# Kernel optimization log

Measured on AMD Instinct MI355X. Metric: run time of the kernel, lower is better.

The kernel has to match this reference:

```python
import jax, jax.numpy as jnp
import numpy as np


def _rms(x, w=None, eps=1e-6):
    # RMSNorm in fp32 like the torch module, optional elementwise affine.
    x32 = x.astype(jnp.float32)
    r = jax.lax.rsqrt(jnp.mean(x32 * x32, axis=-1, keepdims=True) + eps)
    y = (x32 * r).astype(x.dtype)
    return y * w if w is not None else y


def _rotate_half(x):
    x1, x2 = jnp.split(x, 2, axis=-1)
    return jnp.concatenate([-x2, x1], axis=-1)


def setup_inputs() -> dict:
    key = jax.random.key(0)
    ks = jax.random.split(key, 10)
    B, N, C, H = 16, 1024, 1152, 16
    hd = C // H          # 72
    hid = 3072           # _swiglu_hidden(1152, 4.0)
    grid = 32            # grid**2 == N
    quarter = hd // 4    # 18
    # exact axial RoPE cache (build_axial_rope_cache)
    inv_freq = 1.0 / (10000.0 ** (np.arange(quarter, dtype=np.float32) / quarter))
    pos = np.arange(grid, dtype=np.float32)
    f1 = pos[:, None] * inv_freq[None, :]                               # (grid, quarter)
    fy = np.broadcast_to(f1[:, None, :], (grid, grid, quarter)).reshape(-1, quarter)
    fx = np.broadcast_to(f1[None, :, :], (grid, grid, quarter)).reshape(-1, quarter)

    def cs(f):
        e = np.concatenate([f, f], axis=-1)                             # (N, hd//2)
        return jnp.asarray(np.cos(e))[None, None], jnp.asarray(np.sin(e))[None, None]

    cos_y, sin_y = cs(fy)
    cos_x, sin_x = cs(fx)

    def w(k, shp, scale=0.02):
        return jax.random.normal(k, shp, jnp.float32) * scale

    return {
        "x": jax.random.normal(ks[0], (B, N, C), jnp.float32),
        "temb": jax.random.normal(ks[1], (B, C), jnp.float32),
        "cos_y": cos_y, "sin_y": sin_y, "cos_x": cos_x, "sin_x": sin_x,
        "Wqkv": w(ks[2], (3 * C, C)), "bqkv": jnp.zeros((3 * C,), jnp.float32),
        "Wt": w(ks[3], (3 * C, C)), "bt": jnp.zeros((3 * C,), jnp.float32),
        "Wp": w(ks[4], (C, C)), "bp": jnp.zeros((C,), jnp.float32),
        "qn_w": jnp.ones((hd,), jnp.float32), "kn_w": jnp.ones((hd,), jnp.float32),
        "Wg": w(ks[5], (hid, C)), "bg": jnp.zeros((hid,), jnp.float32),
        "Wu": w(ks[6], (hid, C)), "bu": jnp.zeros((hid,), jnp.float32),
        "Wd": w(ks[7], (C, hid)), "bd": jnp.zeros((C,), jnp.float32),
    }


def reference(x, temb, cos_y, sin_y, cos_x, sin_x, Wqkv, bqkv, Wt, bt, Wp, bp,
              qn_w, kn_w, Wg, bg, Wu, bu, Wd, bd):
    B, N, C = x.shape
    H = 16
    hd = C // H

    # --- TMSA attention branch ---
    xn = _rms(x)                                            # norm1 (no affine)
    qkv = xn @ Wqkv.T + bqkv + (temb @ Wt.T + bt)[:, None, :]
    qkv = qkv.reshape(B, N, 3, H, hd).transpose(2, 0, 3, 1, 4)  # (3,B,H,N,hd)
    q, k, v = qkv[0], qkv[1], qkv[2]
    q = _rms(q, qn_w)
    k = _rms(k, kn_w)

    def rope(t):
        ty, tx = jnp.split(t, 2, axis=-1)
        ty = ty * cos_y + _rotate_half(ty) * sin_y
        tx = tx * cos_x + _rotate_half(tx) * sin_x
        return jnp.concatenate([ty, tx], axis=-1)

    q, k = rope(q), rope(k)

    scores = jnp.einsum('bhnd,bhmd->bhnm', q, k) / jnp.sqrt(jnp.float32(hd))
    attn = jax.nn.softmax(scores, axis=-1)
    o = jnp.einsum('bhnm,bhmd->bhnd', attn, v)
    o = o.transpose(0, 2, 1, 3).reshape(B, N, C)
    x = x + (o @ Wp.T + bp)

    # --- SwiGLU MLP branch ---
    xn2 = _rms(x)                                           # norm2 (no affine)
    h = jax.nn.silu(xn2 @ Wg.T + bg) * (xn2 @ Wu.T + bu)
    x = x + (h @ Wd.T + bd)
    return x
```

## Files before the change

kernel.cpp:

```cpp
#include <hip/hip_runtime.h>
#include <cstdint>
#include <cstddef>

typedef unsigned short u16;
typedef unsigned int u32;
typedef __attribute__((ext_vector_type(8))) short bf16x8s;
typedef __attribute__((ext_vector_type(4))) float f32x4;

#define ASG __attribute__((address_space(1)))
#define ASL __attribute__((address_space(3)))

__device__ __forceinline__ u16 f2bf(float f){
  union { float f; unsigned u; } v; v.f = f;
  unsigned r = v.u + 0x7FFFu + ((v.u >> 16) & 1u);
  return (u16)(r >> 16);
}
__device__ __forceinline__ float bf2f(u16 h){
  union { unsigned u; float f; } v; v.u = ((unsigned)h) << 16;
  return v.f;
}

__global__ __launch_bounds__(256) void cvt_kernel(const float* __restrict__ in,
                                                  u16* __restrict__ out, int n){
  int i = blockIdx.x*256 + threadIdx.x;
  if (i < n) out[i] = f2bf(in[i]);
}

__global__ __launch_bounds__(256) void cvt_gu_kernel(const float* __restrict__ Wg,
                                                     const float* __restrict__ Wu,
                                                     u16* __restrict__ out){
  size_t i = (size_t)blockIdx.x*256 + threadIdx.x;
  if (i >= (size_t)6144*1152) return;
  int j = (int)(i / 1152), k = (int)(i % 1152);
  int b16 = j >> 4, w = j & 15;
  int src = (b16 >> 1)*16 + w;
  const float* W = (b16 & 1) ? Wu : Wg;
  out[i] = f2bf(W[(size_t)src*1152 + k]);
}

__global__ __launch_bounds__(256) void temb_kernel(const float* __restrict__ temb,
                                                   const float* __restrict__ Wt,
                                                   const float* __restrict__ bt,
                                                   const float* __restrict__ bqkv,
                                                   float* __restrict__ tvec){
  const int col  = blockIdx.x*4 + (threadIdx.x>>6);
  const int lane = threadIdx.x & 63;
  const float* wp = Wt + (size_t)col*1152;
  float w[18];
  #pragma unroll
  for (int j=0;j<18;j++) w[j] = wp[lane + j*64];
  float acc[16];
  #pragma unroll
  for (int b=0;b<16;b++) acc[b] = 0.f;
  #pragma unroll
  for (int j=0;j<18;j++){
    const int k = lane + j*64;
    #pragma unroll
    for (int b=0;b<16;b++) acc[b] += w[j]*temb[b*1152 + k];
  }
  #pragma unroll
  for (int b=0;b<16;b++){
    #pragma unroll
    for (int d=1; d<64; d<<=1) acc[b] += __shfl_xor(acc[b], d);
  }
  if (lane == 0){
    float add = bt[col] + bqkv[col];
    #pragma unroll
    for (int b=0;b<16;b++) tvec[(size_t)b*3456 + col] = acc[b] + add;
  }
}

__global__ __launch_bounds__(256) void rms_kernel(const float* __restrict__ in,
                                                  u16* __restrict__ out, int C){
  int row = blockIdx.x;
  const float* p = in + (size_t)row*C;
  float ss = 0.f;
  for (int c = threadIdx.x; c < C; c += 256){ float v = p[c]; ss += v*v; }
  #pragma unroll
  for (int d=1; d<64; d<<=1) ss += __shfl_xor(ss, d);
  __shared__ float wsum[4];
  if ((threadIdx.x & 63) == 0) wsum[threadIdx.x>>6] = ss;
  __syncthreads();
  float tot = wsum[0]+wsum[1]+wsum[2]+wsum[3];
  float r = rsqrtf(tot/(float)C + 1e-6f);
  u16* o = out + (size_t)row*C;
  for (int c = threadIdx.x; c < C; c += 256) o[c] = f2bf(p[c]*r);
}

template<int MODE>
__global__ __launch_bounds__(512, 4) void gemm_kernel(
    const u16* __restrict__ A, const u16* __restrict__ B,
    int M, int N, int K, int nbx, int segw,
    const float* __restrict__ bias, const float* __restrict__ fextra,
    void* __restrict__ outv, u16* __restrict__ out2, u16* __restrict__ out3)
{
  __shared__ __align__(16) u16 As0[256*32];
  __shared__ __align__(16) u16 As1[256*32];
  __shared__ __align__(16) u16 As2[256*32];
  __shared__ __align__(16) u16 Bs0[128*32];
  __shared__ __align__(16) u16 Bs1[128*32];
  __shared__ __align__(16) u16 Bs2[128*32];
  const int tid  = threadIdx.x;
  const int lane = tid & 63;
  const int wv   = tid >> 6;
  const int wr   = wv >> 1, wc = wv & 1;

  const int nwg  = (int)gridDim.x;
  const int bid  = (int)blockIdx.x;
  const int xcd  = bid & 7;
  const int slot = bid >> 3;
  const int mdep = (nwg >> 3) / nbx;
  const int segsz = mdep * segw;
  const int seg  = slot / segsz;
  const int rem  = slot - seg*segsz;
  const int mi   = rem / segw;
  const int ni   = seg*segw + (rem - mi*segw);
  const long m0 = (long)(xcd*mdep + mi) * 256;
  const long n0 = (long)ni * 128;

  const u16* Ab = A + (size_t)m0*K;
  const u16* Bb = B + (size_t)n0*K;

  const int gsw  = ((lane&3) ^ ((lane>>3)&3)) * 8;
  const int srow = lane >> 2;

  f32x4 acc[4][4];
  #pragma unroll
  for (int i=0;i<4;i++)
    #pragma unroll
    for (int j=0;j<4;j++) acc[i][j] = (f32x4){0.f,0.f,0.f,0.f};

  auto stage = [&](u16* as, u16* bs, int kt){
    __builtin_amdgcn_global_load_lds(
      (const ASG void*)(Ab + (size_t)(wv*16 + srow)*K + kt + gsw),
      (ASL void*)(as + wv*512), 16, 0, 0);
    __builtin_amdgcn_global_load_lds(
      (const ASG void*)(Ab + (size_t)(128 + wv*16 + srow)*K + kt + gsw),
      (ASL void*)(as + 4096 + wv*512), 16, 0, 0);
    __builtin_amdgcn_global_load_lds(
      (const ASG void*)(Bb + (size_t)(wv*16 + srow)*K + kt + gsw),
      (ASL void*)(bs + wv*512), 16, 0, 0);
  };
  auto compute = [&](const u16* as, const u16* bs){
    const int swc = (((lane>>4) ^ ((lane>>1)&3))) * 8;
    const int lc16 = lane & 15;
    bf16x8s af[4], bfr[4];
    #pragma unroll
    for (int i=0;i<4;i++)
      af[i] = *(const bf16x8s*)(as + (wr*64 + i*16 + lc16)*32 + swc);
    #pragma unroll
    for (int j=0;j<4;j++)
      bfr[j] = *(const bf16x8s*)(bs + (wc*64 + j*16 + lc16)*32 + swc);
    #pragma unroll
    for (int i=0;i<4;i++)
      #pragma unroll
      for (int j=0;j<4;j++)
        acc[i][j] = __builtin_amdgcn_mfma_f32_16x16x32_bf16(af[i], bfr[j], acc[i][j], 0,0,0);
  };

  const int NT = K >> 5;
  stage(As0, Bs0, 0);
  stage(As1, Bs1, 32);
  asm volatile("s_waitcnt vmcnt(3)" ::: "memory");
  __builtin_amdgcn_s_barrier();
  __builtin_amdgcn_sched_barrier(0);

  for (int t = 0; t < NT; t += 3){
    if (t+2 < NT) stage(As2, Bs2, (t+2)*32);
    compute(As0, Bs0);
    if (t+2 < NT) asm volatile("s_waitcnt vmcnt(3)" ::: "memory");
    else          asm volatile("s_waitcnt vmcnt(0)" ::: "memory");
    __builtin_amdgcn_s_barrier();
    __builtin_amdgcn_sched_barrier(0);
    if (t+3 < NT) stage(As0, Bs0, (t+3)*32);
    compute(As1, Bs1);
    if (t+3 < NT) asm volatile("s_waitcnt vmcnt(3)" ::: "memory");
    else          asm volatile("s_waitcnt vmcnt(0)" ::: "memory");
    __builtin_amdgcn_s_barrier();
    __builtin_amdgcn_sched_barrier(0);
    if (t+4 < NT) stage(As1, Bs1, (t+4)*32);
    compute(As2, Bs2);
    if (t+4 < NT) asm volatile("s_waitcnt vmcnt(3)" ::: "memory");
    else          asm volatile("s_waitcnt vmcnt(0)" ::: "memory");
    __builtin_amdgcn_s_barrier();
    __builtin_amdgcn_sched_barrier(0);
  }

  const int lr = (lane>>4)*4, lc = lane&15;
  #pragma unroll
  for (int i=0;i<4;i++){
    #pragma unroll
    for (int j=0;j<4;j++){
      long colg = n0 + wc*64 + j*16 + lc;
      long rowg0 = m0 + wr*64 + i*16 + lr;
      if (MODE==0){
        int cg = (int)colg;
        int which = cg / 1152;
        int rem2 = cg - which*1152;
        int hh = rem2 / 72, dd = rem2 - hh*72;
        int b = (int)(rowg0 >> 10), n = (int)(rowg0 & 1023);
        size_t bh = (size_t)(b*16 + hh);
        float tadd = fextra[(size_t)b*3456 + colg];
        if (which == 2){
          ushort4 vv;
          vv.x = f2bf(acc[i][j][0] + tadd);
          vv.y = f2bf(acc[i][j][1] + tadd);
          vv.z = f2bf(acc[i][j][2] + tadd);
          vv.w = f2bf(acc[i][j][3] + tadd);
          *(ushort4*)(out3 + (bh*72 + dd)*1024 + n) = vv;
        } else {
          u16* dst = (which==0) ? (u16*)outv : out2;
          #pragma unroll
          for (int r=0;r<4;r++)
            dst[(bh*1024 + (size_t)(n + r))*72 + dd] = f2bf(acc[i][j][r] + tadd);
        }
      } else {
        #pragma unroll
        for (int r=0;r<4;r++){
          long rowg = rowg0 + r;
          float v = acc[i][j][r];
          size_t oi = (size_t)rowg*N + colg;
          v += bias[colg] + fextra[oi];
          ((float*)outv)[oi] = v;
        }
      }
    }
  }
}

template<int MODE>
__global__ __launch_bounds__(256, 3) void gemm_half(
    const u16* __restrict__ A, const u16* __restrict__ B,
    int M, int N, int K, int nbx, int segw,
    const float* __restrict__ bias, const float* __restrict__ fextra,
    float* __restrict__ outv)
{
  __shared__ __align__(16) u16 As0[128*32];
  __shared__ __align__(16) u16 As1[128*32];
  __shared__ __align__(16) u16 As2[128*32];
  __shared__ __align__(16) u16 Bs0[128*32];
  __shared__ __align__(16) u16 Bs1[128*32];
  __shared__ __align__(16) u16 Bs2[128*32];
  const int tid  = threadIdx.x;
  const int lane = tid & 63;
  const int wv   = tid >> 6;
  const int wr   = wv >> 1, wc = wv & 1;

  const int nwg  = (int)gridDim.x;
  const int bid  = (int)blockIdx.x;
  const int xcd  = bid & 7;
  const int slot = bid >> 3;
  const int mdep = (nwg >> 3) / nbx;
  const int segsz = mdep * segw;
  const int seg  = slot / segsz;
  const int rem  = slot - seg*segsz;
  const int mi   = rem / segw;
  const int ni   = seg*segw + (rem - mi*segw);
  const long m0 = (long)(xcd*mdep + mi) * 128;
  const long n0 = (long)ni * 128;

  const u16* Ab = A + (size_t)m0*K;
  const u16* Bb = B + (size_t)n0*K;

  const int gsw  = ((lane&3) ^ ((lane>>3)&3)) * 8;
  const int srow = lane >> 2;

  f32x4 acc[4][4];
  #pragma unroll
  for (int i=0;i<4;i++)
    #pragma unroll
    for (int j=0;j<4;j++) acc[i][j] = (f32x4){0.f,0.f,0.f,0.f};

  auto stage = [&](u16* as, u16* bs, int kt){
    __builtin_amdgcn_global_load_lds(
      (const ASG void*)(Ab + (size_t)(wv*16 + srow)*K + kt + gsw),
      (ASL void*)(as + wv*512), 16, 0, 0);
    __builtin_amdgcn_global_load_lds(
      (const ASG void*)(Ab + (size_t)(64 + wv*16 + srow)*K + kt + gsw),
      (ASL void*)(as + 2048 + wv*512), 16, 0, 0);
    __builtin_amdgcn_global_load_lds(
      (const ASG void*)(Bb + (size_t)(wv*16 + srow)*K + kt + gsw),
      (ASL void*)(bs + wv*512), 16, 0, 0);
    __builtin_amdgcn_global_load_lds(
      (const ASG void*)(Bb + (size_t)(64 + wv*16 + srow)*K + kt + gsw),
      (ASL void*)(bs + 2048 + wv*512), 16, 0, 0);
  };
  auto compute = [&](const u16* as, const u16* bs){
    const int swc = (((lane>>4) ^ ((lane>>1)&3))) * 8;
    const int lc16 = lane & 15;
    bf16x8s af[4], bfr[4];
    #pragma unroll
    for (int i=0;i<4;i++)
      af[i] = *(const bf16x8s*)(as + (wr*64 + i*16 + lc16)*32 + swc);
    #pragma unroll
    for (int j=0;j<4;j++)
      bfr[j] = *(const bf16x8s*)(bs + (wc*64 + j*16 + lc16)*32 + swc);
    #pragma unroll
    for (int i=0;i<4;i++)
      #pragma unroll
      for (int j=0;j<4;j++)
        acc[i][j] = __builtin_amdgcn_mfma_f32_16x16x32_bf16(af[i], bfr[j], acc[i][j], 0,0,0);
  };

  const int NT = K >> 5;
  stage(As0, Bs0, 0);
  stage(As1, Bs1, 32);
  asm volatile("s_waitcnt vmcnt(4)" ::: "memory");
  __builtin_amdgcn_s_barrier();
  __builtin_amdgcn_sched_barrier(0);

  for (int t = 0; t < NT; t += 3){
    if (t+2 < NT) stage(As2, Bs2, (t+2)*32);
    compute(As0, Bs0);
    if (t+2 < NT) asm volatile("s_waitcnt vmcnt(4)" ::: "memory");
    else          asm volatile("s_waitcnt vmcnt(0)" ::: "memory");
    __builtin_amdgcn_s_barrier();
    __builtin_amdgcn_sched_barrier(0);
    if (t+3 < NT) stage(As0, Bs0, (t+3)*32);
    compute(As1, Bs1);
    if (t+3 < NT) asm volatile("s_waitcnt vmcnt(4)" ::: "memory");
    else          asm volatile("s_waitcnt vmcnt(0)" ::: "memory");
    __builtin_amdgcn_s_barrier();
    __builtin_amdgcn_sched_barrier(0);
    if (t+4 < NT) stage(As1, Bs1, (t+4)*32);
    compute(As2, Bs2);
    if (t+4 < NT) asm volatile("s_waitcnt vmcnt(4)" ::: "memory");
    else          asm volatile("s_waitcnt vmcnt(0)" ::: "memory");
    __builtin_amdgcn_s_barrier();
    __builtin_amdgcn_sched_barrier(0);
  }

  const int lr = (lane>>4)*4, lc = lane&15;
  #pragma unroll
  for (int i=0;i<4;i++){
    #pragma unroll
    for (int j=0;j<4;j++){
      long colg = n0 + wc*64 + j*16 + lc;
      long rowg0 = m0 + wr*64 + i*16 + lr;
      #pragma unroll
      for (int r=0;r<4;r++){
        long rowg = rowg0 + r;
        size_t oi = (size_t)rowg*N + colg;
        outv[oi] = acc[i][j][r] + bias[colg] + fextra[oi];
      }
    }
  }
}

__global__ __launch_bounds__(512, 2) void gemm_gu8(
    const u16* __restrict__ A, const u16* __restrict__ B,
    int K, int nbx, int segw,
    const float* __restrict__ bg, const float* __restrict__ bu,
    u16* __restrict__ out)
{
  __shared__ __align__(16) u16 As0[256*64];
  __shared__ __align__(16) u16 Bs0[256*64];
  __shared__ __align__(16) u16 As1[256*64];
  __shared__ __align__(16) u16 Bs1[256*64];
  const int tid  = threadIdx.x;
  const int lane = tid & 63;
  const int wv   = tid >> 6;
  const int wr   = wv >> 2;
  const int wc   = wv & 3;
  const int g = lane >> 4, c = lane & 15;

  const int nwg  = (int)gridDim.x;
  const int bid  = (int)blockIdx.x;
  const int xcd  = bid & 7;
  const int slot = bid >> 3;
  const int mdep = (nwg >> 3) / nbx;
  const int segsz = mdep * segw;
  const int seg  = slot / segsz;
  const int rem  = slot - seg*segsz;
  const int mi   = rem / segw;
  const int ni   = seg*segw + (rem - mi*segw);
  const long m0 = (long)(xcd*mdep + mi) * 256;
  const long n0 = (long)ni * 256;

  const u16* Ab = A + (size_t)m0*K;
  const u16* Bb = B + (size_t)n0*K;

  const int srow = tid >> 3;
  const int q8   = ((tid & 7) ^ (srow & 7)) * 8;

  auto stageTo = [&](u16* dst, const u16* src, int h, int kt){
    __builtin_amdgcn_global_load_lds(
      (const ASG void*)(src + (size_t)(h*128 + srow)*K + kt + q8),
      (ASL void*)(dst + h*8192 + wv*512), 16, 0, 0);
    __builtin_amdgcn_global_load_lds(
      (const ASG void*)(src + (size_t)(h*128 + 64 + srow)*K + kt + q8),
      (ASL void*)(dst + h*8192 + 4096 + wv*512), 16, 0, 0);
  };

  f32x4 acc[8][4];
  #pragma unroll
  for (int i=0;i<8;i++)
    #pragma unroll
    for (int j=0;j<4;j++) acc[i][j] = (f32x4){0.f,0.f,0.f,0.f};

  const int sw0 = ((g     ) ^ (c & 7)) * 16;
  const int sw1 = ((4 + g ) ^ (c & 7)) * 16;

  const int NT = K >> 6;

  stageTo(As0, Ab, 0, 0);  stageTo(As0, Ab, 1, 0);
  stageTo(Bs0, Bb, 0, 0);  stageTo(Bs0, Bb, 1, 0);
  stageTo(Bs1, Bb, 0, 64); stageTo(Bs1, Bb, 1, 64);
  asm volatile("s_waitcnt vmcnt(4)" ::: "memory");
  __builtin_amdgcn_s_barrier();
  __builtin_amdgcn_sched_barrier(0);

  auto ktile = [&](const u16* CA, u16* CB, u16* NA, int t){
    const char* aB = (const char*)CA + wr*16384;
    const char* bB = (const char*)CB + (wc>>1)*16384;
    bf16x8s bfr[4][2];
    #pragma unroll
    for (int p=0;p<4;p++){
      const int r0 = (2*p)*16 + c;
      const int r1 = r0 + 16;
      bf16x8s a00 = *(const bf16x8s*)(aB + r0*128 + sw0);
      bf16x8s a01 = *(const bf16x8s*)(aB + r0*128 + sw1);
      bf16x8s a10 = *(const bf16x8s*)(aB + r1*128 + sw0);
      bf16x8s a11 = *(const bf16x8s*)(aB + r1*128 + sw1);
      if (p==0){
        #pragma unroll
        for (int j=0;j<4;j++){
          const int br = (wc&1)*64 + j*16 + c;
          bfr[j][0] = *(const bf16x8s*)(bB + br*128 + sw0);
          bfr[j][1] = *(const bf16x8s*)(bB + br*128 + sw1);
        }
        if (t+1 < NT) stageTo(NA, Ab, 0, (t+1)*64);
      } else if (p==1){
        if (t+1 < NT) stageTo(NA, Ab, 1, (t+1)*64);
      } else if (p==2){
        if (t+2 < NT) stageTo(CB, Bb, 0, (t+2)*64);
      } else {
        if (t+2 < NT) stageTo(CB, Bb, 1, (t+2)*64);
      }
      __builtin_amdgcn_s_barrier();
      asm volatile("s_waitcnt lgkmcnt(0)" ::: "memory");
      __builtin_amdgcn_sched_barrier(0);
      __builtin_amdgcn_s_setprio(1);
      #pragma unroll
      for (int j=0;j<4;j++){
        acc[2*p  ][j] = __builtin_amdgcn_mfma_f32_16x16x32_bf16(a00, bfr[j][0], acc[2*p  ][j],0,0,0);
        acc[2*p  ][j] = __builtin_amdgcn_mfma_f32_16x16x32_bf16(a01, bfr[j][1], acc[2*p  ][j],0,0,0);
        acc[2*p+1][j] = __builtin_amdgcn_mfma_f32_16x16x32_bf16(a10, bfr[j][0], acc[2*p+1][j],0,0,0);
        acc[2*p+1][j] = __builtin_amdgcn_mfma_f32_16x16x32_bf16(a11, bfr[j][1], acc[2*p+1][j],0,0,0);
      }
      __builtin_amdgcn_s_setprio(0);
      if (p==3){
        if (t+2 < NT) asm volatile("s_waitcnt vmcnt(4)" ::: "memory");
        else          asm volatile("s_waitcnt vmcnt(0)" ::: "memory");
      }
      __builtin_amdgcn_s_barrier();
      __builtin_amdgcn_sched_barrier(0);
    }
  };

  for (int tp = 0; tp < NT; tp += 2){
    ktile(As0, Bs0, As1, tp);
    ktile(As1, Bs1, As0, tp+1);
  }

  #pragma unroll
  for (int i=0;i<8;i++){
    #pragma unroll
    for (int jp=0;jp<2;jp++){
      long hcol = (n0>>1) + wc*32 + jp*16 + c;
      float bgv = bg[hcol], buv = bu[hcol];
      #pragma unroll
      for (int r=0;r<4;r++){
        long rowg = m0 + wr*128 + i*16 + g*4 + r;
        float gv = acc[i][2*jp  ][r] + bgv;
        float uv = acc[i][2*jp+1][r] + buv;
        float hv = (gv/(1.f + __expf(-gv))) * uv;
        out[(size_t)rowg*3072 + hcol] = f2bf(hv);
      }
    }
  }
}

__global__ __launch_bounds__(256) void qkrope_kernel(
    u16* __restrict__ Q, u16* __restrict__ K,
    const float* __restrict__ qn_w, const float* __restrict__ kn_w,
    const float* __restrict__ cos_y, const float* __restrict__ sin_y,
    const float* __restrict__ cos_x, const float* __restrict__ sin_x)
{
  const int gw   = blockIdx.x*4 + (threadIdx.x>>6);
  const int lane = threadIdx.x & 63;
  const int n = gw & 1023;
  const int d0 = lane*2;
  const bool act = d0 < 72;
  const float scale = 0.11785113019775793f;

  u16* qp = Q + (size_t)gw*72;
  u16* kp = K + (size_t)gw*72;
  float q0=0,q1=0,k0=0,k1=0,wq0=0,wq1=0,wk0=0,wk1=0;
  if (act){
    q0 = bf2f(qp[d0]); q1 = bf2f(qp[d0+1]);
    k0 = bf2f(kp[d0]); k1 = bf2f(kp[d0+1]);
    wq0 = qn_w[d0]; wq1 = qn_w[d0+1];
    wk0 = kn_w[d0]; wk1 = kn_w[d0+1];
  }
  float ssq = q0*q0 + q1*q1;
  float ssk = k0*k0 + k1*k1;
  #pragma unroll
  for (int d=1; d<64; d<<=1){ ssq += __shfl_xor(ssq,d); ssk += __shfl_xor(ssk,d); }
  const float rq = rsqrtf(ssq*(1.f/72.f) + 1e-6f);
  const float rk = rsqrtf(ssk*(1.f/72.f) + 1e-6f);
  float qn0 = q0*rq*wq0, qn1 = q1*rq*wq1;
  float kn0 = k0*rk*wk0, kn1 = k1*rk*wk1;

  int dh = d0 % 36;
  const bool first = (dh < 18);
  int partner = first ? lane+9 : lane-9;
  if (!act) partner = lane;
  float pq0 = __shfl(qn0, partner), pq1 = __shfl(qn1, partner);
  float pk0 = __shfl(kn0, partner), pk1 = __shfl(kn1, partner);
  if (act){
    const float* cp = (d0 < 36) ? cos_y : cos_x;
    const float* sp = (d0 < 36) ? sin_y : sin_x;
    float c0 = cp[n*36+dh], c1 = cp[n*36+dh+1];
    float s0 = sp[n*36+dh], s1 = sp[n*36+dh+1];
    float sgn = first ? -1.f : 1.f;
    float qo0 = (qn0*c0 + sgn*pq0*s0)*scale, qo1 = (qn1*c1 + sgn*pq1*s1)*scale;
    float ko0 = kn0*c0 + sgn*pk0*s0,         ko1 = kn1*c1 + sgn*pk1*s1;
    *(unsigned*)(qp + d0) = (unsigned)f2bf(qo0) | ((unsigned)f2bf(qo1)<<16);
    *(unsigned*)(kp + d0) = (unsigned)f2bf(ko0) | ((unsigned)f2bf(ko1)<<16);
  }
}

__global__ __launch_bounds__(256, 3) void attn_kernel(
    const u16* __restrict__ Q, const u16* __restrict__ K,
    const u16* __restrict__ Vt, u16* __restrict__ O)
{
  const int tid  = threadIdx.x;
  const int lane = tid & 63;
  const int wv   = tid >> 6;
  const int g = lane >> 4, c = lane & 15;
  const int bid  = blockIdx.x;
  const int head = (bid >> 6) * 8 + (bid & 7);
  const int q0   = ((bid >> 3) & 7) * 128;
  const int b = head >> 4, h = head & 15;

  __shared__ __align__(16) u16 Vlds[80][72];
  __shared__ __align__(16) u16 Plds[8][16][64];

  const bf16x8s zf = {0,0,0,0,0,0,0,0};
  const u16* Kp = K + (size_t)head*1024*72;
  const u16* Qb = Q + ((size_t)head*1024 + q0 + wv*32)*72;
  const char* Vg = (const char*)(Vt + (size_t)head*72*1024);

  bf16x8s qf[2][3];
  #pragma unroll
  for (int s=0;s<2;s++){
    const u16* qrow = Qb + (size_t)(s*16 + c)*72;
    qf[s][0] = *(const bf16x8s*)(qrow + g*8);
    qf[s][1] = *(const bf16x8s*)(qrow + 32 + g*8);
    qf[s][2] = (g==0) ? *(const bf16x8s*)(qrow + 64) : zf;
  }

  f32x4 oacc[2][5];
  float lsum[2] = {0.f, 0.f};
  #pragma unroll
  for (int s=0;s<2;s++)
    #pragma unroll
    for (int c5=0;c5<5;c5++) oacc[s][c5] = (f32x4){0.f,0.f,0.f,0.f};

  char* pb0 = (char*)Plds + (wv*2+0)*2048 + c*128;
  char* pb1 = pb0 + 2048;
  const int swz = (c & 7) << 4;

  int4 vr0, vr1, vr2;
  {
    vr0 = *(const int4*)(Vg + ((tid    )>>3)*2048 + ((tid    )&7)*16);
    vr1 = *(const int4*)(Vg + ((256+tid)>>3)*2048 + ((256+tid)&7)*16);
    if (tid < 64) vr2 = *(const int4*)(Vg + ((512+tid)>>3)*2048 + ((512+tid)&7)*16);
  }
  if (tid < 288) ((u32*)&Vlds[72][0])[tid] = 0u;
  {
    *(int4*)((char*)Vlds + ((tid    )>>3)*144 + ((tid    )&7)*16) = vr0;
    *(int4*)((char*)Vlds + ((256+tid)>>3)*144 + ((256+tid)&7)*16) = vr1;
    if (tid < 64) *(int4*)((char*)Vlds + ((512+tid)>>3)*144 + ((512+tid)&7)*16) = vr2;
  }

  for (int t = 0; t < 16; ++t){
    const int kv0 = t*64;
    __syncthreads();
    if (t < 15){
      const char* vs = Vg + (kv0+64)*2;
      vr0 = *(const int4*)(vs + ((tid    )>>3)*2048 + ((tid    )&7)*16);
      vr1 = *(const int4*)(vs + ((256+tid)>>3)*2048 + ((256+tid)&7)*16);
      if (tid < 64) vr2 = *(const int4*)(vs + ((512+tid)>>3)*2048 + ((512+tid)&7)*16);
    }

    #pragma unroll
    for (int nf=0; nf<4; nf++){
      const u16* krow = Kp + (size_t)(kv0 + nf*16 + c)*72;
      bf16x8s kf0 = *(const bf16x8s*)(krow + g*8);
      bf16x8s kf1 = *(const bf16x8s*)(krow + 32 + g*8);
      bf16x8s kf2 = (g==0) ? *(const bf16x8s*)(krow + 64) : zf;
      #pragma unroll
      for (int s=0;s<2;s++){
        f32x4 sc = (f32x4){0.f,0.f,0.f,0.f};
        sc = __builtin_amdgcn_mfma_f32_16x16x32_bf16(kf0, qf[s][0], sc,0,0,0);
        sc = __builtin_amdgcn_mfma_f32_16x16x32_bf16(kf1, qf[s][1], sc,0,0,0);
        sc = __builtin_amdgcn_mfma_f32_16x16x32_bf16(kf2, qf[s][2], sc,0,0,0);
        float p0 = __expf(sc[0]), p1 = __expf(sc[1]);
        float p2 = __expf(sc[2]), p3 = __expf(sc[3]);
        lsum[s] += (p0+p1) + (p2+p3);
        u32 w0 = (u32)f2bf(p0) | ((u32)f2bf(p1) << 16);
        u32 w1 = (u32)f2bf(p2) | ((u32)f2bf(p3) << 16);
        char* pb = s ? pb1 : pb0;
        int kb = nf*32 + g*8;
        *(u32*)(pb + ( kb      ^ swz)) = w0;
        *(u32*)(pb + ((kb + 4) ^ swz)) = w1;
      }
    }
    asm volatile("" ::: "memory");
    bf16x8s pa[2][2];
    #pragma unroll
    for (int s=0;s<2;s++)
      #pragma unroll
      for (int w2=0;w2<2;w2++)
        pa[s][w2] = *(const bf16x8s*)((s?pb1:pb0) + ((w2*64 + g*16) ^ swz));

    #pragma unroll
    for (int c5=0;c5<5;c5++){
      #pragma unroll
      for (int w2=0;w2<2;w2++){
        bf16x8s vf = *(const bf16x8s*)((const char*)Vlds + (size_t)(c5*16+c)*144 + w2*64 + g*16);
        oacc[0][c5] = __builtin_amdgcn_mfma_f32_16x16x32_bf16(pa[0][w2], vf, oacc[0][c5],0,0,0);
        oacc[1][c5] = __builtin_amdgcn_mfma_f32_16x16x32_bf16(pa[1][w2], vf, oacc[1][c5],0,0,0);
      }
    }

    if (t < 15){
      __syncthreads();
      *(int4*)((char*)Vlds + ((tid    )>>3)*144 + ((tid    )&7)*16) = vr0;
      *(int4*)((char*)Vlds + ((256+tid)>>3)*144 + ((256+tid)&7)*16) = vr1;
      if (tid < 64) *(int4*)((char*)Vlds + ((512+tid)>>3)*144 + ((512+tid)&7)*16) = vr2;
    }
  }

  size_t obase = (size_t)b*1024*1152 + (size_t)h*72;
  #pragma unroll
  for (int s=0;s<2;s++){
    float ls = lsum[s];
    ls += __shfl_xor(ls, 16);
    ls += __shfl_xor(ls, 32);
    float linv[4];
    #pragma unroll
    for (int r=0;r<4;r++) linv[r] = 1.0f / __shfl(ls, 4*g + r);
    #pragma unroll
    for (int c5=0;c5<5;c5++){
      int d = c5*16 + c;
      if (d < 72){
        #pragma unroll
        for (int r=0;r<4;r++){
          int n = q0 + wv*32 + s*16 + 4*g + r;
          O[obase + (size_t)n*1152 + d] = f2bf(oacc[s][c5][r]*linv[r]);
        }
      }
    }
  }
}

extern "C" void kernel_launch(void* const* d_in, const int* in_sizes, int n_in,
                              void* d_out, int out_size, void* d_ws, size_t ws_size,
                              hipStream_t stream) {
  const float* x    = (const float*)d_in[0];
  const float* temb = (const float*)d_in[1];
  const float* cos_y= (const float*)d_in[2];
  const float* sin_y= (const float*)d_in[3];
  const float* cos_x= (const float*)d_in[4];
  const float* sin_x= (const float*)d_in[5];
  const float* Wqkv = (const float*)d_in[6];
  const float* bqkv = (const float*)d_in[7];
  const float* Wt   = (const float*)d_in[8];
  const float* bt   = (const float*)d_in[9];
  const float* Wp   = (const float*)d_in[10];
  const float* bp   = (const float*)d_in[11];
  const float* qn_w = (const float*)d_in[12];
  const float* kn_w = (const float*)d_in[13];
  const float* Wg   = (const float*)d_in[14];
  const float* bg   = (const float*)d_in[15];
  const float* Wu   = (const float*)d_in[16];
  const float* bu   = (const float*)d_in[17];
  const float* Wd   = (const float*)d_in[18];
  const float* bd   = (const float*)d_in[19];

  char* ws = (char*)d_ws;
  size_t off = 0;
  auto alloc = [&](size_t bytes)->void*{
    off = (off + 255) & ~(size_t)255;
    void* p = ws + off; off += bytes; return p;
  };

  u16*   wbuf  = (u16*)alloc((size_t)6144*1152*2);
  float* tvec  = (float*)alloc((size_t)16*3456*4);
  u16*   xn_bf = (u16*)alloc((size_t)16384*1152*2);
  u16*   qt    = (u16*)alloc((size_t)262144*72*2);
  u16*   kt    = (u16*)alloc((size_t)262144*72*2);
  u16*   vt    = (u16*)alloc((size_t)256*72*1024*2);
  if (off > ws_size) return;

  u16*   o_bf   = xn_bf;
  u16*   xn2_bf = xn_bf;
  u16*   gbuf   = qt;
  float* x1     = (float*)d_out;

  rms_kernel<<<16384,256,0,stream>>>(x, xn_bf, 1152);
  temb_kernel<<<864,256,0,stream>>>(temb, Wt, bt, bqkv, tvec);

  cvt_kernel<<<(3456*1152+255)/256,256,0,stream>>>(Wqkv, wbuf, 3456*1152);
  gemm_kernel<0><<<64*27,512,0,stream>>>(
      xn_bf, wbuf, 16384, 3456, 1152, 27, 9, nullptr, tvec, qt, kt, vt);

  qkrope_kernel<<<65536,256,0,stream>>>(qt, kt, qn_w, kn_w, cos_y, sin_y, cos_x, sin_x);

  attn_kernel<<<2048,256,0,stream>>>(qt, kt, vt, o_bf);

  cvt_kernel<<<(1152*1152+255)/256,256,0,stream>>>(Wp, wbuf, 1152*1152);
  gemm_half<1><<<128*9,256,0,stream>>>(
      o_bf, wbuf, 16384, 1152, 1152, 9, 9, bp, x, x1);

  rms_kernel<<<16384,256,0,stream>>>(x1, xn2_bf, 1152);

  cvt_gu_kernel<<<(6144*1152+255)/256,256,0,stream>>>(Wg, Wu, wbuf);
  gemm_gu8<<<1536,512,0,stream>>>(
      xn2_bf, wbuf, 1152, 24, 4, bg, bu, gbuf);

  cvt_kernel<<<(1152*3072+255)/256,256,0,stream>>>(Wd, wbuf, 1152*3072);
  gemm_half<4><<<128*9,256,0,stream>>>(
      gbuf, wbuf, 16384, 1152, 3072, 9, 3, bd, x1, (float*)d_out);
}
```

Before: 983.6 us.

## Vectorize weight conversion and RMSNorm, restructure gate-up GEMM k-tile schedule

The fp32-to-bf16 weight conversion kernels and the RMSNorm kernel now use float4 loads and ushort4 stores. RMSNorm also keeps each row in registers so it is read from global memory only once. The gate/up GEMM k-tile loop changes from four barrier-separated phases to two larger MFMA batches with fewer barriers, and it issues more LDS loads before compute. The intent is to cut memory-instruction count and synchronisation overhead, at the cost of higher register pressure in the GEMM.

Result: faster. 922.9 us (median of 2 runs) (-6.2%).

```diff
diff --git a/kernel.cpp b/kernel.cpp
--- a/kernel.cpp
+++ b/kernel.cpp
@@ -21,21 +21,27 @@
 }
 
 __global__ __launch_bounds__(256) void cvt_kernel(const float* __restrict__ in,
-                                                  u16* __restrict__ out, int n){
+                                                  u16* __restrict__ out, int n4){
   int i = blockIdx.x*256 + threadIdx.x;
-  if (i < n) out[i] = f2bf(in[i]);
+  if (i < n4){
+    float4 v = ((const float4*)in)[i];
+    ushort4 o; o.x = f2bf(v.x); o.y = f2bf(v.y); o.z = f2bf(v.z); o.w = f2bf(v.w);
+    ((ushort4*)out)[i] = o;
+  }
 }
 
 __global__ __launch_bounds__(256) void cvt_gu_kernel(const float* __restrict__ Wg,
                                                      const float* __restrict__ Wu,
                                                      u16* __restrict__ out){
-  size_t i = (size_t)blockIdx.x*256 + threadIdx.x;
-  if (i >= (size_t)6144*1152) return;
-  int j = (int)(i / 1152), k = (int)(i % 1152);
+  int i4 = blockIdx.x*256 + threadIdx.x;
+  if (i4 >= 6144*288) return;
+  int j = i4 / 288, k4 = i4 - j*288;
   int b16 = j >> 4, w = j & 15;
   int src = (b16 >> 1)*16 + w;
   const float* W = (b16 & 1) ? Wu : Wg;
-  out[i] = f2bf(W[(size_t)src*1152 + k]);
+  float4 v = ((const float4*)W)[(size_t)src*288 + k4];
+  ushort4 o; o.x = f2bf(v.x); o.y = f2bf(v.y); o.z = f2bf(v.z); o.w = f2bf(v.w);
+  ((ushort4*)out)[i4] = o;
 }
 
 __global__ __launch_bounds__(256) void temb_kernel(const float* __restrict__ temb,
@@ -72,19 +78,28 @@
 
 __global__ __launch_bounds__(256) void rms_kernel(const float* __restrict__ in,
                                                   u16* __restrict__ out, int C){
-  int row = blockIdx.x;
-  const float* p = in + (size_t)row*C;
-  float ss = 0.f;
-  for (int c = threadIdx.x; c < C; c += 256){ float v = p[c]; ss += v*v; }
+  const int tid = threadIdx.x;
+  const int row = blockIdx.x;
+  const float4* p4 = (const float4*)(in + (size_t)row*1152);
+  float4 v0 = p4[tid];
+  float4 v1 = {0.f,0.f,0.f,0.f};
+  if (tid < 32) v1 = p4[256 + tid];
+  float ss = v0.x*v0.x + v0.y*v0.y + v0.z*v0.z + v0.w*v0.w
+           + v1.x*v1.x + v1.y*v1.y + v1.z*v1.z + v1.w*v1.w;
   #pragma unroll
   for (int d=1; d<64; d<<=1) ss += __shfl_xor(ss, d);
   __shared__ float wsum[4];
-  if ((threadIdx.x & 63) == 0) wsum[threadIdx.x>>6] = ss;
+  if ((tid & 63) == 0) wsum[tid>>6] = ss;
   __syncthreads();
   float tot = wsum[0]+wsum[1]+wsum[2]+wsum[3];
-  float r = rsqrtf(tot/(float)C + 1e-6f);
-  u16* o = out + (size_t)row*C;
-  for (int c = threadIdx.x; c < C; c += 256) o[c] = f2bf(p[c]*r);
+  float r = rsqrtf(tot*(1.f/1152.f) + 1e-6f);
+  ushort4* o4 = (ushort4*)(out + (size_t)row*1152);
+  ushort4 o; o.x=f2bf(v0.x*r); o.y=f2bf(v0.y*r); o.z=f2bf(v0.z*r); o.w=f2bf(v0.w*r);
+  o4[tid] = o;
+  if (tid < 32){
+    ushort4 o1; o1.x=f2bf(v1.x*r); o1.y=f2bf(v1.y*r); o1.z=f2bf(v1.z*r); o1.w=f2bf(v1.w*r);
+    o4[256+tid] = o1;
+  }
 }
 
 template<int MODE>
@@ -413,49 +428,56 @@
   auto ktile = [&](const u16* CA, u16* CB, u16* NA, int t){
     const char* aB = (const char*)CA + wr*16384;
     const char* bB = (const char*)CB + (wc>>1)*16384;
-    bf16x8s bfr[4][2];
-    #pragma unroll
-    for (int p=0;p<4;p++){
-      const int r0 = (2*p)*16 + c;
-      const int r1 = r0 + 16;
-      bf16x8s a00 = *(const bf16x8s*)(aB + r0*128 + sw0);
-      bf16x8s a01 = *(const bf16x8s*)(aB + r0*128 + sw1);
-      bf16x8s a10 = *(const bf16x8s*)(aB + r1*128 + sw0);
-      bf16x8s a11 = *(const bf16x8s*)(aB + r1*128 + sw1);
-      if (p==0){
-        #pragma unroll
-        for (int j=0;j<4;j++){
-          const int br = (wc&1)*64 + j*16 + c;
-          bfr[j][0] = *(const bf16x8s*)(bB + br*128 + sw0);
-          bfr[j][1] = *(const bf16x8s*)(bB + br*128 + sw1);
-        }
-        if (t+1 < NT) stageTo(NA, Ab, 0, (t+1)*64);
-      } else if (p==1){
-        if (t+1 < NT) stageTo(NA, Ab, 1, (t+1)*64);
-      } else if (p==2){
-        if (t+2 < NT) stageTo(CB, Bb, 0, (t+2)*64);
-      } else {
-        if (t+2 < NT) stageTo(CB, Bb, 1, (t+2)*64);
+    bf16x8s bfr[4][2], a0[4][2];
+    #pragma unroll
+    for (int j=0;j<4;j++){
+      const int br = (wc&1)*64 + j*16 + c;
+      bfr[j][0] = *(const bf16x8s*)(bB + br*128 + sw0);
+      bfr[j][1] = *(const bf16x8s*)(bB + br*128 + sw1);
+    }
+    #pragma unroll
+    for (int i=0;i<4;i++){
+      const int ar = i*16 + c;
+      a0[i][0] = *(const bf16x8s*)(aB + ar*128 + sw0);
+      a0[i][1] = *(const bf16x8s*)(aB + ar*128 + sw1);
+    }
+    if (t+1 < NT){ stageTo(NA, Ab, 0, (t+1)*64); stageTo(NA, Ab, 1, (t+1)*64); }
+    asm volatile("s_waitcnt lgkmcnt(0)" ::: "memory");
+    __builtin_amdgcn_sched_barrier(0);
+    __builtin_amdgcn_s_barrier();
+    if (t+2 < NT) stageTo(CB, Bb, 0, (t+2)*64);
+    __builtin_amdgcn_s_setprio(1);
+    #pragma unroll
+    for (int i=0;i<4;i++)
+      #pragma unroll
+      for (int j=0;j<4;j++){
+        acc[i][j] = __builtin_amdgcn_mfma_f32_16x16x32_bf16(a0[i][0], bfr[j][0], acc[i][j],0,0,0);
+        acc[i][j] = __builtin_amdgcn_mfma_f32_16x16x32_bf16(a0[i][1], bfr[j][1], acc[i][j],0,0,0);
       }
-      __builtin_amdgcn_s_barrier();
-      asm volatile("s_waitcnt lgkmcnt(0)" ::: "memory");
-      __builtin_amdgcn_sched_barrier(0);
-      __builtin_amdgcn_s_setprio(1);
+    __builtin_amdgcn_s_setprio(0);
+    bf16x8s a1[4][2];
+    #pragma unroll
+    for (int i=0;i<4;i++){
+      const int ar = (4+i)*16 + c;
+      a1[i][0] = *(const bf16x8s*)(aB + ar*128 + sw0);
+      a1[i][1] = *(const bf16x8s*)(aB + ar*128 + sw1);
+    }
+    if (t+2 < NT) stageTo(CB, Bb, 1, (t+2)*64);
+    asm volatile("s_waitcnt lgkmcnt(0)" ::: "memory");
+    __builtin_amdgcn_sched_barrier(0);
+    __builtin_amdgcn_s_setprio(1);
+    #pragma unroll
+    for (int i=0;i<4;i++)
       #pragma unroll
       for (int j=0;j<4;j++){
-        acc[2*p  ][j] = __builtin_amdgcn_mfma_f32_16x16x32_bf16(a00, bfr[j][0], acc[2*p  ][j],0,0,0);
-        acc[2*p  ][j] = __builtin_amdgcn_mfma_f32_16x16x32_bf16(a01, bfr[j][1], acc[2*p  ][j],0,0,0);
-        acc[2*p+1][j] = __builtin_amdgcn_mfma_f32_16x16x32_bf16(a10, bfr[j][0], acc[2*p+1][j],0,0,0);
-        acc[2*p+1][j] = __builtin_amdgcn_mfma_f32_16x16x32_bf16(a11, bfr[j][1], acc[2*p+1][j],0,0,0);
+        acc[4+i][j] = __builtin_amdgcn_mfma_f32_16x16x32_bf16(a1[i][0], bfr[j][0], acc[4+i][j],0,0,0);
+        acc[4+i][j] = __builtin_amdgcn_mfma_f32_16x16x32_bf16(a1[i][1], bfr[j][1], acc[4+i][j],0,0,0);
       }
-      __builtin_amdgcn_s_setprio(0);
-      if (p==3){
-        if (t+2 < NT) asm volatile("s_waitcnt vmcnt(4)" ::: "memory");
-        else          asm volatile("s_waitcnt vmcnt(0)" ::: "memory");
-      }
-      __builtin_amdgcn_s_barrier();
-      __builtin_amdgcn_sched_barrier(0);
-    }
+    __builtin_amdgcn_s_setprio(0);
+    if (t+2 < NT) asm volatile("s_waitcnt vmcnt(4)" ::: "memory");
+    else          asm volatile("s_waitcnt vmcnt(0)" ::: "memory");
+    __builtin_amdgcn_s_barrier();
+    __builtin_amdgcn_sched_barrier(0);
   };
 
   for (int tp = 0; tp < NT; tp += 2){
@@ -714,7 +736,7 @@
   rms_kernel<<<16384,256,0,stream>>>(x, xn_bf, 1152);
   temb_kernel<<<864,256,0,stream>>>(temb, Wt, bt, bqkv, tvec);
 
-  cvt_kernel<<<(3456*1152+255)/256,256,0,stream>>>(Wqkv, wbuf, 3456*1152);
+  cvt_kernel<<<(3456*288+255)/256,256,0,stream>>>(Wqkv, wbuf, 3456*288);
   gemm_kernel<0><<<64*27,512,0,stream>>>(
       xn_bf, wbuf, 16384, 3456, 1152, 27, 9, nullptr, tvec, qt, kt, vt);
 
@@ -722,17 +744,17 @@
 
   attn_kernel<<<2048,256,0,stream>>>(qt, kt, vt, o_bf);
 
-  cvt_kernel<<<(1152*1152+255)/256,256,0,stream>>>(Wp, wbuf, 1152*1152);
+  cvt_kernel<<<(1152*288+255)/256,256,0,stream>>>(Wp, wbuf, 1152*288);
   gemm_half<1><<<128*9,256,0,stream>>>(
       o_bf, wbuf, 16384, 1152, 1152, 9, 9, bp, x, x1);
 
   rms_kernel<<<16384,256,0,stream>>>(x1, xn2_bf, 1152);
 
-  cvt_gu_kernel<<<(6144*1152+255)/256,256,0,stream>>>(Wg, Wu, wbuf);
+  cvt_gu_kernel<<<(6144*288+255)/256,256,0,stream>>>(Wg, Wu, wbuf);
   gemm_gu8<<<1536,512,0,stream>>>(
       xn2_bf, wbuf, 1152, 24, 4, bg, bu, gbuf);
 
-  cvt_kernel<<<(1152*3072+255)/256,256,0,stream>>>(Wd, wbuf, 1152*3072);
+  cvt_kernel<<<(3072*288+255)/256,256,0,stream>>>(Wd, wbuf, 3072*288);
   gemm_half<4><<<128*9,256,0,stream>>>(
       gbuf, wbuf, 16384, 1152, 3072, 9, 3, bd, x1, (float*)d_out);
 }
```
